# Optimization experiments

Measured on AMD Instinct MI355X. Metric: run time of the kernel, lower is better.

The kernel has to match this reference:

```python
import jax, jax.numpy as jnp
import numpy as np

B, V, FIN, K, FOUT, E = 8, 100000, 32, 4, 64, 800000


def setup_inputs() -> dict:
    key = jax.random.key(0)
    ks = jax.random.split(key, 6)
    inputs = jax.random.normal(ks[0], (B, V, FIN), dtype=jnp.float32)
    lap_rows = jax.random.randint(ks[1], (E,), 0, V, dtype=jnp.int32)
    lap_cols = jax.random.randint(ks[2], (E,), 0, V, dtype=jnp.int32)
    # rescaled-Laplacian nonzeros; small magnitude keeps the Chebyshev recurrence stable
    lap_vals = jax.random.normal(ks[3], (E,), dtype=jnp.float32) * 0.1
    # Kaiming-normal init: std = sqrt(2 / (Fin * K)) as in reset_parameters()
    std = float(np.sqrt(2.0 / (FIN * K)))
    weight = jax.random.normal(ks[4], (FIN, K, FOUT), dtype=jnp.float32) * std
    bias = jax.random.normal(ks[5], (FOUT,), dtype=jnp.float32) * 0.01
    return dict(inputs=inputs, lap_rows=lap_rows, lap_cols=lap_cols,
                lap_vals=lap_vals, weight=weight, bias=bias)


def reference(inputs, lap_rows, lap_cols, lap_vals, weight, bias):
    # inputs: [B, V, Fin]; weight: [Fin, K, Fout]; Laplacian in COO form.
    Bn, Vn, Fin = inputs.shape
    _, Kn, Fout = weight.shape

    def spmm(x):  # x: [V, Fin, B] -> L @ x via gather + segment-sum over edges
        msgs = lap_vals[:, None, None] * x[lap_cols]  # [E, Fin, B]
        return jax.ops.segment_sum(msgs, lap_rows, num_segments=Vn)

    x0 = jnp.transpose(inputs, (1, 2, 0))  # [V, Fin, B]
    xs = [x0]
    if Kn > 1:
        x1 = spmm(x0)
        xs.append(x1)
    for _ in range(2, Kn):
        x2 = 2.0 * spmm(x1) - x0  # Chebyshev recurrence T_k = 2 L T_{k-1} - T_{k-2}
        xs.append(x2)
        x0, x1 = x1, x2
    x = jnp.stack(xs, axis=0)  # [K, V, Fin, B]
    out = jnp.einsum('kvfb,fko->bvo', x, weight) + bias  # [B, V, Fout]
    return out
```

## Files before the change

kernel.cpp:

```cpp
#include <hip/hip_runtime.h>
#include <hip/hip_bf16.h>

#define B_    8
#define V_    100000
#define FIN_  32
#define K_    4
#define FOUT_ 64
#define E_    800000
#define NODE_F 256

typedef __attribute__((ext_vector_type(8))) short bf16x8;
typedef __attribute__((ext_vector_type(4))) float floatx4;

static __device__ inline float bf2f(unsigned short u) {
    unsigned int x = ((unsigned int)u) << 16;
    return __builtin_bit_cast(float, x);
}
static __device__ inline unsigned short f2bf(float f) {
    __hip_bfloat16 h = __float2bfloat16(f);
    return __builtin_bit_cast(unsigned short, h);
}

__global__ __launch_bounds__(256) void k_transpose(const float* __restrict__ in,
                                                   unsigned short* __restrict__ x0,
                                                   const int* __restrict__ rows,
                                                   int* __restrict__ counts,
                                                   const float* __restrict__ weight,
                                                   unsigned short* __restrict__ wpack) {
    int tid = blockIdx.x * 256 + threadIdx.x;
    int f4 = tid & 7;
    int m  = tid >> 3;
    int v  = m >> 3;
    int b  = m & 7;
    float4 val = ((const float4*)(in + ((size_t)b * V_ + v) * FIN_))[f4];
    ushort4 o;
    o.x = f2bf(val.x); o.y = f2bf(val.y); o.z = f2bf(val.z); o.w = f2bf(val.w);
    ((ushort4*)x0)[tid] = o;

    if (tid < E_) atomicAdd(&counts[rows[tid]], 1);

    if (tid < 1024) {
        int lane = tid & 63;
        int ot   = (tid >> 6) & 3;
        int kq   = tid >> 8;
        int quad = lane >> 4, l16 = lane & 15;
        bf16x8 w;
        #pragma unroll
        for (int j = 0; j < 8; ++j)
            w[j] = (short)f2bf(weight[(size_t)(quad * 8 + j) * (K_ * FOUT_) + kq * FOUT_ + ot * 16 + l16]);
        *((bf16x8*)(wpack + (size_t)tid * 8)) = w;
    }
}

__global__ __launch_bounds__(256) void k_zero_int(int* __restrict__ p, int n) {
    int t = blockIdx.x * 256 + threadIdx.x;
    if (t < n) p[t] = 0;
}

__global__ __launch_bounds__(1024) void k_scan1(const int* __restrict__ counts,
                                                int* __restrict__ row_ptr,
                                                int* __restrict__ cursor,
                                                int* __restrict__ bsums, int n) {
    __shared__ int s[1024];
    int t = threadIdx.x;
    int idx = blockIdx.x * 1024 + t;
    int v = (idx < n) ? counts[idx] : 0;
    s[t] = v;
    __syncthreads();
    for (int off = 1; off < 1024; off <<= 1) {
        int add = (t >= off) ? s[t - off] : 0;
        __syncthreads();
        s[t] += add;
        __syncthreads();
    }
    if (idx < n) {
        int r = s[t] - v;
        row_ptr[idx] = r;
        cursor[idx]  = r;
    }
    if (t == 1023) bsums[blockIdx.x] = s[1023];
}

__global__ __launch_bounds__(128) void k_scan2(const int* __restrict__ bsums,
                                               int* __restrict__ boffs, int nb) {
    __shared__ int s[128];
    int t = threadIdx.x;
    int v = (t < nb) ? bsums[t] : 0;
    s[t] = v;
    __syncthreads();
    for (int off = 1; off < 128; off <<= 1) {
        int add = (t >= off) ? s[t - off] : 0;
        __syncthreads();
        s[t] += add;
        __syncthreads();
    }
    boffs[t] = s[t] - v;
}

__global__ __launch_bounds__(256) void k_scatter(const int* __restrict__ rows,
                                                 const int* __restrict__ cols,
                                                 const float* __restrict__ vals,
                                                 int* __restrict__ cursor,
                                                 const int* __restrict__ boffs,
                                                 int2* __restrict__ e_pack) {
    int e = blockIdx.x * 256 + threadIdx.x;
    if (e < E_) {
        int r = rows[e];
        int pos = atomicAdd(&cursor[r], 1) + boffs[r >> 10];
        e_pack[pos] = make_int2(cols[e], __float_as_int(vals[e]));
    }
}

__global__ __launch_bounds__(256) void k_spmm(const unsigned short* __restrict__ xc,
                                              const unsigned short* __restrict__ xp,
                                              const int* __restrict__ row_ptr,
                                              const int* __restrict__ boffs,
                                              const int2* __restrict__ ep,
                                              unsigned short* __restrict__ xn,
                                              float scale, int has_prev) {
    int wave = threadIdx.x >> 6;
    int lane = threadIdx.x & 63;
    int half = lane >> 5;
    int hl   = lane & 31;
    int v = blockIdx.x * 4 + wave;
    if (v >= V_) return;
    int beg = row_ptr[v] + boffs[v >> 10];
    int end = (v == V_ - 1) ? E_ : row_ptr[v + 1] + boffs[(v + 1) >> 10];

    float acc[8] = {0.f, 0.f, 0.f, 0.f, 0.f, 0.f, 0.f, 0.f};
    int e = beg + half;
    for (; e + 6 < end; e += 8) {
        int2 p0 = ep[e];
        int2 p1 = ep[e + 2];
        int2 p2 = ep[e + 4];
        int2 p3 = ep[e + 6];
        bf16x8 g0 = *((const bf16x8*)(xc + (size_t)p0.x * NODE_F + hl * 8));
        bf16x8 g1 = *((const bf16x8*)(xc + (size_t)p1.x * NODE_F + hl * 8));
        bf16x8 g2 = *((const bf16x8*)(xc + (size_t)p2.x * NODE_F + hl * 8));
        bf16x8 g3 = *((const bf16x8*)(xc + (size_t)p3.x * NODE_F + hl * 8));
        float v0 = __int_as_float(p0.y);
        float v1 = __int_as_float(p1.y);
        float v2 = __int_as_float(p2.y);
        float v3 = __int_as_float(p3.y);
        #pragma unroll
        for (int j = 0; j < 8; ++j) acc[j] += v0 * bf2f((unsigned short)g0[j]);
        #pragma unroll
        for (int j = 0; j < 8; ++j) acc[j] += v1 * bf2f((unsigned short)g1[j]);
        #pragma unroll
        for (int j = 0; j < 8; ++j) acc[j] += v2 * bf2f((unsigned short)g2[j]);
        #pragma unroll
        for (int j = 0; j < 8; ++j) acc[j] += v3 * bf2f((unsigned short)g3[j]);
    }
    for (; e + 2 < end; e += 4) {
        int2 p0 = ep[e];
        int2 p1 = ep[e + 2];
        bf16x8 g0 = *((const bf16x8*)(xc + (size_t)p0.x * NODE_F + hl * 8));
        bf16x8 g1 = *((const bf16x8*)(xc + (size_t)p1.x * NODE_F + hl * 8));
        float v0 = __int_as_float(p0.y);
        float v1 = __int_as_float(p1.y);
        #pragma unroll
        for (int j = 0; j < 8; ++j) acc[j] += v0 * bf2f((unsigned short)g0[j]);
        #pragma unroll
        for (int j = 0; j < 8; ++j) acc[j] += v1 * bf2f((unsigned short)g1[j]);
    }
    for (; e < end; e += 2) {
        int2 p = ep[e];
        bf16x8 g = *((const bf16x8*)(xc + (size_t)p.x * NODE_F + hl * 8));
        float vv = __int_as_float(p.y);
        #pragma unroll
        for (int j = 0; j < 8; ++j) acc[j] += vv * bf2f((unsigned short)g[j]);
    }

    #pragma unroll
    for (int j = 0; j < 8; ++j) acc[j] += __shfl_xor(acc[j], 32);

    if (half == 0) {
        float r[8];
        if (has_prev) {
            bf16x8 p = *((const bf16x8*)(xp + (size_t)v * NODE_F + hl * 8));
            #pragma unroll
            for (int j = 0; j < 8; ++j) r[j] = scale * acc[j] - bf2f((unsigned short)p[j]);
        } else {
            #pragma unroll
            for (int j = 0; j < 8; ++j) r[j] = acc[j];
        }
        bf16x8 o;
        #pragma unroll
        for (int j = 0; j < 8; ++j) o[j] = (short)f2bf(r[j]);
        *((bf16x8*)(xn + (size_t)v * NODE_F + hl * 8)) = o;
    }
}

#define TILES_PER_WAVE 5
__global__ __launch_bounds__(256) void k_contract(const unsigned short* __restrict__ x0,
                                                  const unsigned short* __restrict__ x1,
                                                  const unsigned short* __restrict__ x2,
                                                  const unsigned short* __restrict__ x3,
                                                  const unsigned short* __restrict__ wpack,
                                                  const float* __restrict__ bias,
                                                  float* __restrict__ out) {
    int wave = threadIdx.x >> 6;
    int lane = threadIdx.x & 63;
    int quad = lane >> 4;
    int l16  = lane & 15;
    const unsigned short* xs[4] = {x0, x1, x2, x3};

    bf16x8 wfrag[4][4];
    #pragma unroll
    for (int kq = 0; kq < 4; ++kq)
        #pragma unroll
        for (int ot = 0; ot < 4; ++ot)
            wfrag[kq][ot] = *((const bf16x8*)(wpack + (size_t)((kq * 4 + ot) * 64 + lane) * 8));

    floatx4 bi[4];
    #pragma unroll
    for (int ot = 0; ot < 4; ++ot)
        bi[ot] = *((const floatx4*)(bias + ot * 16 + quad * 4));

    int wid   = blockIdx.x * 4 + wave;
    int tile0 = wid * TILES_PER_WAVE;
    #pragma unroll 1
    for (int t = 0; t < TILES_PER_WAVE; ++t) {
        int m0 = (tile0 + t) * 16;
        floatx4 acc[4] = {bi[0], bi[1], bi[2], bi[3]};
        #pragma unroll
        for (int kq = 0; kq < 4; ++kq) {
            bf16x8 xf = *((const bf16x8*)(xs[kq] + (size_t)(m0 + l16) * FIN_ + quad * 8));
            #pragma unroll
            for (int ot = 0; ot < 4; ++ot)
                acc[ot] = __builtin_amdgcn_mfma_f32_16x16x32_bf16(wfrag[kq][ot], xf, acc[ot], 0, 0, 0);
        }
        int m = m0 + l16;
        int v = m >> 3;
        int b = m & 7;
        float* op = out + ((size_t)b * V_ + v) * FOUT_ + quad * 4;
        #pragma unroll
        for (int ot = 0; ot < 4; ++ot)
            *((floatx4*)(op + ot * 16)) = acc[ot];
    }
}

extern "C" void kernel_launch(void* const* d_in, const int* in_sizes, int n_in,
                              void* d_out, int out_size, void* d_ws, size_t ws_size,
                              hipStream_t stream) {
    const float* inputs  = (const float*)d_in[0];
    const int*   laprows = (const int*)d_in[1];
    const int*   lapcols = (const int*)d_in[2];
    const float* lapvals = (const float*)d_in[3];
    const float* weight  = (const float*)d_in[4];
    const float* bias    = (const float*)d_in[5];
    float* out = (float*)d_out;

    const size_t XN = (size_t)V_ * NODE_F;
    unsigned short* x0 = (unsigned short*)d_ws;
    unsigned short* x1 = x0 + XN;
    unsigned short* x2 = x1 + XN;
    unsigned short* x3 = x2 + XN;
    int* counts  = (int*)(x3 + XN);
    int* row_ptr = counts + V_;
    int* cursor  = row_ptr + V_;
    int* bsums   = cursor + V_;
    int* boffs   = bsums + 128;
    int2* e_pack = (int2*)(boffs + 128);
    unsigned short* wpack = (unsigned short*)(e_pack + E_);

    const int NB_SCAN = (V_ + 1023) / 1024;

    hipLaunchKernelGGL(k_zero_int, dim3((V_ + 255) / 256), dim3(256), 0, stream, counts, V_);
    hipLaunchKernelGGL(k_transpose, dim3((V_ * B_ * 8) / 256), dim3(256), 0, stream,
                       inputs, x0, laprows, counts, weight, wpack);
    hipLaunchKernelGGL(k_scan1, dim3(NB_SCAN), dim3(1024), 0, stream,
                       counts, row_ptr, cursor, bsums, V_);
    hipLaunchKernelGGL(k_scan2, dim3(1), dim3(128), 0, stream, bsums, boffs, NB_SCAN);
    hipLaunchKernelGGL(k_scatter, dim3((E_ + 255) / 256), dim3(256), 0, stream,
                       laprows, lapcols, lapvals, cursor, boffs, e_pack);

    hipLaunchKernelGGL(k_spmm, dim3(V_ / 4), dim3(256), 0, stream,
                       x0, (const unsigned short*)nullptr, row_ptr, boffs, e_pack, x1, 1.0f, 0);
    hipLaunchKernelGGL(k_spmm, dim3(V_ / 4), dim3(256), 0, stream,
                       x1, x0, row_ptr, boffs, e_pack, x2, 2.0f, 1);
    hipLaunchKernelGGL(k_spmm, dim3(V_ / 4), dim3(256), 0, stream,
                       x2, x1, row_ptr, boffs, e_pack, x3, 2.0f, 1);

    hipLaunchKernelGGL(k_contract, dim3(2500), dim3(256), 0, stream,
                       x0, x1, x2, x3, wpack, bias, out);
}
```

Baseline: 626.5 us.

## Fuse last Chebyshev SpMM into MFMA contraction and use full-wave per-row gathers

The third SpMM step is fused into the contraction kernel. Each wave computes two rows of x3 into shared memory and then runs the MFMA contraction on them directly, so the x3 buffer is never written to or read from global memory and one launch is removed. The SpMM inner loop also changes from two half-waves each gathering 16-byte chunks to a full wave gathering 8-byte chunks per edge. This means fewer bytes per load instruction and no cross-half reduction. The trade-off is a fused kernel with a __syncthreads and less streaming work per wave in the contraction.

```diff
diff --git a/kernel.cpp b/kernel.cpp
--- a/kernel.cpp
+++ b/kernel.cpp
@@ -111,6 +111,31 @@
     }
 }
 
+static __device__ inline void spmm_row(const unsigned short* __restrict__ xc,
+                                       const int2* __restrict__ ep,
+                                       int beg, int end, int lane, float a[4]) {
+    int e = beg;
+    for (; e + 3 < end; e += 4) {
+        int2 p0 = ep[e], p1 = ep[e + 1], p2 = ep[e + 2], p3 = ep[e + 3];
+        ushort4 g0 = *((const ushort4*)(xc + (size_t)p0.x * NODE_F + lane * 4));
+        ushort4 g1 = *((const ushort4*)(xc + (size_t)p1.x * NODE_F + lane * 4));
+        ushort4 g2 = *((const ushort4*)(xc + (size_t)p2.x * NODE_F + lane * 4));
+        ushort4 g3 = *((const ushort4*)(xc + (size_t)p3.x * NODE_F + lane * 4));
+        float w0 = __int_as_float(p0.y), w1 = __int_as_float(p1.y);
+        float w2 = __int_as_float(p2.y), w3 = __int_as_float(p3.y);
+        a[0] += w0 * bf2f(g0.x); a[1] += w0 * bf2f(g0.y); a[2] += w0 * bf2f(g0.z); a[3] += w0 * bf2f(g0.w);
+        a[0] += w1 * bf2f(g1.x); a[1] += w1 * bf2f(g1.y); a[2] += w1 * bf2f(g1.z); a[3] += w1 * bf2f(g1.w);
+        a[0] += w2 * bf2f(g2.x); a[1] += w2 * bf2f(g2.y); a[2] += w2 * bf2f(g2.z); a[3] += w2 * bf2f(g2.w);
+        a[0] += w3 * bf2f(g3.x); a[1] += w3 * bf2f(g3.y); a[2] += w3 * bf2f(g3.z); a[3] += w3 * bf2f(g3.w);
+    }
+    for (; e < end; ++e) {
+        int2 p = ep[e];
+        ushort4 g = *((const ushort4*)(xc + (size_t)p.x * NODE_F + lane * 4));
+        float w = __int_as_float(p.y);
+        a[0] += w * bf2f(g.x); a[1] += w * bf2f(g.y); a[2] += w * bf2f(g.z); a[3] += w * bf2f(g.w);
+    }
+}
+
 __global__ __launch_bounds__(256) void k_spmm(const unsigned short* __restrict__ xc,
                                               const unsigned short* __restrict__ xp,
                                               const int* __restrict__ row_ptr,
@@ -120,91 +145,64 @@
                                               float scale, int has_prev) {
     int wave = threadIdx.x >> 6;
     int lane = threadIdx.x & 63;
-    int half = lane >> 5;
-    int hl   = lane & 31;
     int v = blockIdx.x * 4 + wave;
     if (v >= V_) return;
     int beg = row_ptr[v] + boffs[v >> 10];
     int end = (v == V_ - 1) ? E_ : row_ptr[v + 1] + boffs[(v + 1) >> 10];
 
-    float acc[8] = {0.f, 0.f, 0.f, 0.f, 0.f, 0.f, 0.f, 0.f};
-    int e = beg + half;
-    for (; e + 6 < end; e += 8) {
-        int2 p0 = ep[e];
-        int2 p1 = ep[e + 2];
-        int2 p2 = ep[e + 4];
-        int2 p3 = ep[e + 6];
-        bf16x8 g0 = *((const bf16x8*)(xc + (size_t)p0.x * NODE_F + hl * 8));
-        bf16x8 g1 = *((const bf16x8*)(xc + (size_t)p1.x * NODE_F + hl * 8));
-        bf16x8 g2 = *((const bf16x8*)(xc + (size_t)p2.x * NODE_F + hl * 8));
-        bf16x8 g3 = *((const bf16x8*)(xc + (size_t)p3.x * NODE_F + hl * 8));
-        float v0 = __int_as_float(p0.y);
-        float v1 = __int_as_float(p1.y);
-        float v2 = __int_as_float(p2.y);
-        float v3 = __int_as_float(p3.y);
-        #pragma unroll
-        for (int j = 0; j < 8; ++j) acc[j] += v0 * bf2f((unsigned short)g0[j]);
-        #pragma unroll
-        for (int j = 0; j < 8; ++j) acc[j] += v1 * bf2f((unsigned short)g1[j]);
-        #pragma unroll
-        for (int j = 0; j < 8; ++j) acc[j] += v2 * bf2f((unsigned short)g2[j]);
-        #pragma unroll
-        for (int j = 0; j < 8; ++j) acc[j] += v3 * bf2f((unsigned short)g3[j]);
-    }
-    for (; e + 2 < end; e += 4) {
-        int2 p0 = ep[e];
-        int2 p1 = ep[e + 2];
-        bf16x8 g0 = *((const bf16x8*)(xc + (size_t)p0.x * NODE_F + hl * 8));
-        bf16x8 g1 = *((const bf16x8*)(xc + (size_t)p1.x * NODE_F + hl * 8));
-        float v0 = __int_as_float(p0.y);
-        float v1 = __int_as_float(p1.y);
-        #pragma unroll
-        for (int j = 0; j < 8; ++j) acc[j] += v0 * bf2f((unsigned short)g0[j]);
-        #pragma unroll
-        for (int j = 0; j < 8; ++j) acc[j] += v1 * bf2f((unsigned short)g1[j]);
-    }
-    for (; e < end; e += 2) {
-        int2 p = ep[e];
-        bf16x8 g = *((const bf16x8*)(xc + (size_t)p.x * NODE_F + hl * 8));
-        float vv = __int_as_float(p.y);
-        #pragma unroll
-        for (int j = 0; j < 8; ++j) acc[j] += vv * bf2f((unsigned short)g[j]);
-    }
-
-    #pragma unroll
-    for (int j = 0; j < 8; ++j) acc[j] += __shfl_xor(acc[j], 32);
-
-    if (half == 0) {
-        float r[8];
-        if (has_prev) {
-            bf16x8 p = *((const bf16x8*)(xp + (size_t)v * NODE_F + hl * 8));
-            #pragma unroll
-            for (int j = 0; j < 8; ++j) r[j] = scale * acc[j] - bf2f((unsigned short)p[j]);
-        } else {
-            #pragma unroll
-            for (int j = 0; j < 8; ++j) r[j] = acc[j];
-        }
-        bf16x8 o;
-        #pragma unroll
-        for (int j = 0; j < 8; ++j) o[j] = (short)f2bf(r[j]);
-        *((bf16x8*)(xn + (size_t)v * NODE_F + hl * 8)) = o;
-    }
-}
-
-#define TILES_PER_WAVE 5
-__global__ __launch_bounds__(256) void k_contract(const unsigned short* __restrict__ x0,
-                                                  const unsigned short* __restrict__ x1,
-                                                  const unsigned short* __restrict__ x2,
-                                                  const unsigned short* __restrict__ x3,
-                                                  const unsigned short* __restrict__ wpack,
-                                                  const float* __restrict__ bias,
-                                                  float* __restrict__ out) {
+    float a[4] = {0.f, 0.f, 0.f, 0.f};
+    spmm_row(xc, ep, beg, end, lane, a);
+
+    float r[4];
+    if (has_prev) {
+        ushort4 p = *((const ushort4*)(xp + (size_t)v * NODE_F + lane * 4));
+        r[0] = scale * a[0] - bf2f(p.x);
+        r[1] = scale * a[1] - bf2f(p.y);
+        r[2] = scale * a[2] - bf2f(p.z);
+        r[3] = scale * a[3] - bf2f(p.w);
+    } else {
+        r[0] = a[0]; r[1] = a[1]; r[2] = a[2]; r[3] = a[3];
+    }
+    ushort4 o;
+    o.x = f2bf(r[0]); o.y = f2bf(r[1]); o.z = f2bf(r[2]); o.w = f2bf(r[3]);
+    *((ushort4*)(xn + (size_t)v * NODE_F + lane * 4)) = o;
+}
+
+__global__ __launch_bounds__(256) void k_spmm3c(const unsigned short* __restrict__ x0,
+                                                const unsigned short* __restrict__ x1,
+                                                const unsigned short* __restrict__ x2,
+                                                const int* __restrict__ row_ptr,
+                                                const int* __restrict__ boffs,
+                                                const int2* __restrict__ ep,
+                                                const unsigned short* __restrict__ wpack,
+                                                const float* __restrict__ bias,
+                                                float* __restrict__ out) {
+    __shared__ __align__(16) unsigned short x3s[4][2][NODE_F];
     int wave = threadIdx.x >> 6;
     int lane = threadIdx.x & 63;
     int quad = lane >> 4;
     int l16  = lane & 15;
-    const unsigned short* xs[4] = {x0, x1, x2, x3};
-
+    int pair = blockIdx.x * 4 + wave;
+    int v0 = pair * 2;
+
+    #pragma unroll 1
+    for (int s = 0; s < 2; ++s) {
+        int v = v0 + s;
+        int beg = row_ptr[v] + boffs[v >> 10];
+        int end = (v == V_ - 1) ? E_ : row_ptr[v + 1] + boffs[(v + 1) >> 10];
+        float a[4] = {0.f, 0.f, 0.f, 0.f};
+        spmm_row(x2, ep, beg, end, lane, a);
+        ushort4 p1 = *((const ushort4*)(x1 + (size_t)v * NODE_F + lane * 4));
+        ushort4 o;
+        o.x = f2bf(2.f * a[0] - bf2f(p1.x));
+        o.y = f2bf(2.f * a[1] - bf2f(p1.y));
+        o.z = f2bf(2.f * a[2] - bf2f(p1.z));
+        o.w = f2bf(2.f * a[3] - bf2f(p1.w));
+        *((ushort4*)&x3s[wave][s][lane * 4]) = o;
+    }
+    __syncthreads();
+
+    const unsigned short* xs012[3] = {x0, x1, x2};
     bf16x8 wfrag[4][4];
     #pragma unroll
     for (int kq = 0; kq < 4; ++kq)
@@ -212,32 +210,31 @@
         for (int ot = 0; ot < 4; ++ot)
             wfrag[kq][ot] = *((const bf16x8*)(wpack + (size_t)((kq * 4 + ot) * 64 + lane) * 8));
 
-    floatx4 bi[4];
+    floatx4 acc[4];
     #pragma unroll
     for (int ot = 0; ot < 4; ++ot)
-        bi[ot] = *((const floatx4*)(bias + ot * 16 + quad * 4));
-
-    int wid   = blockIdx.x * 4 + wave;
-    int tile0 = wid * TILES_PER_WAVE;
-    #pragma unroll 1
-    for (int t = 0; t < TILES_PER_WAVE; ++t) {
-        int m0 = (tile0 + t) * 16;
-        floatx4 acc[4] = {bi[0], bi[1], bi[2], bi[3]};
-        #pragma unroll
-        for (int kq = 0; kq < 4; ++kq) {
-            bf16x8 xf = *((const bf16x8*)(xs[kq] + (size_t)(m0 + l16) * FIN_ + quad * 8));
-            #pragma unroll
-            for (int ot = 0; ot < 4; ++ot)
-                acc[ot] = __builtin_amdgcn_mfma_f32_16x16x32_bf16(wfrag[kq][ot], xf, acc[ot], 0, 0, 0);
-        }
-        int m = m0 + l16;
-        int v = m >> 3;
-        int b = m & 7;
-        float* op = out + ((size_t)b * V_ + v) * FOUT_ + quad * 4;
+        acc[ot] = *((const floatx4*)(bias + ot * 16 + quad * 4));
+
+    int m0 = pair * 16;
+    #pragma unroll
+    for (int kq = 0; kq < 4; ++kq) {
+        bf16x8 xf;
+        if (kq < 3)
+            xf = *((const bf16x8*)(xs012[kq] + (size_t)(m0 + l16) * FIN_ + quad * 8));
+        else
+            xf = *((const bf16x8*)&x3s[wave][l16 >> 3][(l16 & 7) * FIN_ + quad * 8]);
         #pragma unroll
         for (int ot = 0; ot < 4; ++ot)
-            *((floatx4*)(op + ot * 16)) = acc[ot];
-    }
+            acc[ot] = __builtin_amdgcn_mfma_f32_16x16x32_bf16(wfrag[kq][ot], xf, acc[ot], 0, 0, 0);
+    }
+
+    int m = m0 + l16;
+    int v = m >> 3;
+    int b = m & 7;
+    float* op = out + ((size_t)b * V_ + v) * FOUT_ + quad * 4;
+    #pragma unroll
+    for (int ot = 0; ot < 4; ++ot)
+        *((floatx4*)(op + ot * 16)) = acc[ot];
 }
 
 extern "C" void kernel_launch(void* const* d_in, const int* in_sizes, int n_in,
@@ -255,8 +252,7 @@
     unsigned short* x0 = (unsigned short*)d_ws;
     unsigned short* x1 = x0 + XN;
     unsigned short* x2 = x1 + XN;
-    unsigned short* x3 = x2 + XN;
-    int* counts  = (int*)(x3 + XN);
+    int* counts  = (int*)(x2 + XN);
     int* row_ptr = counts + V_;
     int* cursor  = row_ptr + V_;
     int* bsums   = cursor + V_;
@@ -279,9 +275,7 @@
                        x0, (const unsigned short*)nullptr, row_ptr, boffs, e_pack, x1, 1.0f, 0);
     hipLaunchKernelGGL(k_spmm, dim3(V_ / 4), dim3(256), 0, stream,
                        x1, x0, row_ptr, boffs, e_pack, x2, 2.0f, 1);
-    hipLaunchKernelGGL(k_spmm, dim3(V_ / 4), dim3(256), 0, stream,
-                       x2, x1, row_ptr, boffs, e_pack, x3, 2.0f, 1);
-
-    hipLaunchKernelGGL(k_contract, dim3(2500), dim3(256), 0, stream,
-                       x0, x1, x2, x3, wpack, bias, out);
-}
+
+    hipLaunchKernelGGL(k_spmm3c, dim3(12500), dim3(256), 0, stream,
+                       x0, x1, x2, row_ptr, boffs, e_pack, wpack, bias, out);
+}
```

Result: faster. 608.8 us (-2.8%).
